# Performance work log

Measured on AMD Instinct MI355X. Metric: run time of the kernel, lower is better.

Reference implementation:

```python
import jax, jax.numpy as jnp
import numpy as np

ALPHA = 0.01  # matches LineFinderLoss(alpha=0.01)


def setup_inputs() -> dict:
    key = jax.random.key(0)
    k1, k2 = jax.random.split(key)
    S = 4096  # square so N == M == S (required for the original code to run)
    # column 4 is used as a probability: log(c) and log(1-c) must be finite
    inp = jax.random.uniform(k1, (S, S), dtype=jnp.float32, minval=1e-4, maxval=1.0 - 1e-4)
    tgt = jax.random.uniform(k2, (S, S), dtype=jnp.float32)
    return {"input": inp, "target": tgt}


def reference(input, target):
    N = input.shape[1]
    M = target.shape[1]
    # pairwise MSE cost over the first two coordinates: cost[n,m] = mean((input[n,:2]-target[m,:2])^2)
    diff = input[:, None, 0:2] - target[None, :, 0:2]  # [N, M, 2]
    cost = jnp.mean(diff * diff, axis=-1)              # [N, M]
    # Hungarian on an NxN cost yields a full assignment; the original code sets
    # X[p,l]=1 for the OUTER PRODUCT of matched row/col index sets, so X == ones
    # deterministically (matching does not affect the output).
    X = jnp.ones((N, M), dtype=input.dtype)
    mse_full = jnp.mean((input - target) ** 2)  # self.mse(input, target), constant over (n,m)
    log_c = jnpp_log = jnp.log(input[:, 4])     # [N]
    log_1mc = jnp.log(1.0 - input[:, 4])        # [N]
    # sum_{n,m} X*(alpha*mse_full - log c_n) - (1-X)*log(1-c_n)
    term = X * (ALPHA * mse_full - log_c[:, None]) - (1.0 - X) * log_1mc[:, None]
    # torch mse_loss(input[:,3], target) broadcasts (S,) against (S,S): elem [i,j] = (input[j,3]-target[i,j])^2
    loss = jnp.sum(term) + jnp.mean((input[:, 3] - target) ** 2)
    return loss, cost
```

## Files before the change

### kernel.cpp

```cpp
#include <hip/hip_runtime.h>

#define SDIM 4096
#define ALPHA 0.01f
#define WS_LOG 8
#define WS_ARR 128
#define WS_PART (WS_ARR + 5 * SDIM)


__global__ void k_gather(const float* __restrict__ inp, const float* __restrict__ tgt,
                         float* __restrict__ ws) {
    int n = blockIdx.x * 64 + threadIdx.x;
    const float* row = inp + (size_t)n * SDIM;
    const float* trow = tgt + (size_t)n * SDIM;
    float* arr = ws + WS_ARR;

    float v0 = row[0], v1 = row[1], v3 = row[3], v4 = row[4];
    arr[n]            = v0;
    arr[SDIM + n]     = v1;
    arr[2 * SDIM + n] = v3;
    arr[3 * SDIM + n] = trow[0];
    arr[4 * SDIM + n] = trow[1];

    float lg = logf(v4);
    #pragma unroll
    for (int off = 32; off > 0; off >>= 1) lg += __shfl_down(lg, off);
    if (threadIdx.x == 0) ws[WS_LOG + blockIdx.x] = lg;
}

__global__ void __launch_bounds__(256) k_main(const float* __restrict__ inp,
                                              const float* __restrict__ tgt,
                                              const float* __restrict__ ws,
                                              float* __restrict__ out,
                                              float* __restrict__ wpart) {
    __shared__ float s1[4], s2[4];
    const float* c0 = ws + WS_ARR;
    const float* c1 = c0 + SDIM;
    const float* c3 = c0 + 2 * SDIM;
    const float* t0 = c0 + 3 * SDIM;
    const float* t1 = c0 + 4 * SDIM;

    int n = blockIdx.x;
    int t = threadIdx.x;
    const float* irow = inp + (size_t)n * SDIM;
    const float* trow = tgt + (size_t)n * SDIM;
    float* orow = out + 1 + (size_t)n * SDIM;

    float4 vi[4], vt[4];
    #pragma unroll
    for (int k = 0; k < 4; ++k) {
        int col = (k * 256 + t) * 4;
        vi[k] = *(const float4*)(irow + col);
        vt[k] = *(const float4*)(trow + col);
    }
    float4 vc[4], w0[4], w1[4];
    #pragma unroll
    for (int k = 0; k < 4; ++k) {
        int col = (k * 256 + t) * 4;
        vc[k] = *(const float4*)(c3 + col);
        w0[k] = *(const float4*)(t0 + col);
        w1[k] = *(const float4*)(t1 + col);
    }
    float a0 = c0[n];
    float b0 = c1[n];

    float a1 = 0.0f, a2 = 0.0f;
    #pragma unroll
    for (int k = 0; k < 4; ++k) {
        int col = (k * 256 + t) * 4;
        float d, e0, e1;
        d = vi[k].x - vt[k].x; a1 += d * d;
        d = vi[k].y - vt[k].y; a1 += d * d;
        d = vi[k].z - vt[k].z; a1 += d * d;
        d = vi[k].w - vt[k].w; a1 += d * d;
        d = vc[k].x - vt[k].x; a2 += d * d;
        d = vc[k].y - vt[k].y; a2 += d * d;
        d = vc[k].z - vt[k].z; a2 += d * d;
        d = vc[k].w - vt[k].w; a2 += d * d;
        e0 = a0 - w0[k].x; e1 = b0 - w1[k].x; orow[col + 0] = 0.5f * (e0 * e0 + e1 * e1);
        e0 = a0 - w0[k].y; e1 = b0 - w1[k].y; orow[col + 1] = 0.5f * (e0 * e0 + e1 * e1);
        e0 = a0 - w0[k].z; e1 = b0 - w1[k].z; orow[col + 2] = 0.5f * (e0 * e0 + e1 * e1);
        e0 = a0 - w0[k].w; e1 = b0 - w1[k].w; orow[col + 3] = 0.5f * (e0 * e0 + e1 * e1);
    }

    #pragma unroll
    for (int off = 32; off > 0; off >>= 1) {
        a1 += __shfl_down(a1, off);
        a2 += __shfl_down(a2, off);
    }
    int wave = t >> 6;
    if ((t & 63) == 0) { s1[wave] = a1; s2[wave] = a2; }
    __syncthreads();
    if (t == 0) {
        wpart[n]        = s1[0] + s1[1] + s1[2] + s1[3];
        wpart[SDIM + n] = s2[0] + s2[1] + s2[2] + s2[3];
    }
}

__global__ void k_final(const float* __restrict__ ws, float* __restrict__ out) {
    __shared__ float s1[4], s2[4];
    float a1 = 0.0f, a2 = 0.0f;
    const float* wpart = ws + WS_PART;
    for (int i = threadIdx.x; i < SDIM; i += 256) {
        a1 += wpart[i];
        a2 += wpart[SDIM + i];
    }
    #pragma unroll
    for (int off = 32; off > 0; off >>= 1) {
        a1 += __shfl_down(a1, off);
        a2 += __shfl_down(a2, off);
    }
    int wave = threadIdx.x >> 6;
    if ((threadIdx.x & 63) == 0) { s1[wave] = a1; s2[wave] = a2; }
    __syncthreads();
    if (threadIdx.x == 0) {
        float sum_sq = s1[0] + s1[1] + s1[2] + s1[3];
        float sum3   = s2[0] + s2[1] + s2[2] + s2[3];
        float slog = 0.0f;
        #pragma unroll
        for (int i = 0; i < 64; ++i) slog += ws[WS_LOG + i];
        out[0] = ALPHA * sum_sq - (float)SDIM * slog
               + sum3 * (1.0f / ((float)SDIM * (float)SDIM));
    }
}

extern "C" void kernel_launch(void* const* d_in, const int* in_sizes, int n_in,
                              void* d_out, int out_size, void* d_ws, size_t ws_size,
                              hipStream_t stream) {
    const float* inp = (const float*)d_in[0];
    const float* tgt = (const float*)d_in[1];
    float* out = (float*)d_out;
    float* ws  = (float*)d_ws;

    k_gather<<<64, 64, 0, stream>>>(inp, tgt, ws);
    k_main<<<SDIM, 256, 0, stream>>>(inp, tgt, ws, out, ws + WS_PART);
    k_final<<<1, 256, 0, stream>>>(ws, out);
}
```

Baseline: 181.4 us.

## Split main kernel into reduction blocks and aligned float4 cost-row writer blocks

Replaces the single per-row kernel with a grid that interleaves reduction blocks (every third block, reading input/target in large strided float4 chunks) and cost-writer blocks. The writer blocks store the output shifted by one element so each row is written with aligned float4 stores. This handles the off-by-one offset of the cost matrix within the output buffer by pre-shifting the target columns in the gather kernel and patching the boundary elements. The aim is to replace scalar unaligned stores with vector stores and to separate read-heavy work from write-heavy work. The cost is more complex indexing and special-case boundary handling.

New measurement: 185.4 us. 1.02x slower.

```diff
diff --git a/kernel.cpp b/kernel.cpp
--- a/kernel.cpp
+++ b/kernel.cpp
@@ -5,12 +5,13 @@
 #define WS_LOG 8
 #define WS_ARR 128
 #define WS_PART (WS_ARR + 5 * SDIM)
+#define NRED 2048
 
 
 __global__ void k_gather(const float* __restrict__ inp, const float* __restrict__ tgt,
                          float* __restrict__ ws) {
     int n = blockIdx.x * 64 + threadIdx.x;
-    const float* row = inp + (size_t)n * SDIM;
+    const float* row  = inp + (size_t)n * SDIM;
     const float* trow = tgt + (size_t)n * SDIM;
     float* arr = ws + WS_ARR;
 
@@ -18,8 +19,9 @@
     arr[n]            = v0;
     arr[SDIM + n]     = v1;
     arr[2 * SDIM + n] = v3;
-    arr[3 * SDIM + n] = trow[0];
-    arr[4 * SDIM + n] = trow[1];
+    int ns = (n + 1) & (SDIM - 1);
+    arr[3 * SDIM + ns] = trow[0];
+    arr[4 * SDIM + ns] = trow[1];
 
     float lg = logf(v4);
     #pragma unroll
@@ -27,72 +29,86 @@
     if (threadIdx.x == 0) ws[WS_LOG + blockIdx.x] = lg;
 }
 
-__global__ void __launch_bounds__(256) k_main(const float* __restrict__ inp,
-                                              const float* __restrict__ tgt,
-                                              const float* __restrict__ ws,
-                                              float* __restrict__ out,
-                                              float* __restrict__ wpart) {
+__global__ void __launch_bounds__(256) k_fused(const float* __restrict__ inp,
+                                               const float* __restrict__ tgt,
+                                               const float* __restrict__ ws,
+                                               float* __restrict__ out,
+                                               float* __restrict__ wpart) {
     __shared__ float s1[4], s2[4];
+    int bid = blockIdx.x;
+    int t = threadIdx.x;
     const float* c0 = ws + WS_ARR;
-    const float* c1 = c0 + SDIM;
-    const float* c3 = c0 + 2 * SDIM;
-    const float* t0 = c0 + 3 * SDIM;
-    const float* t1 = c0 + 4 * SDIM;
 
-    int n = blockIdx.x;
-    int t = threadIdx.x;
-    const float* irow = inp + (size_t)n * SDIM;
-    const float* trow = tgt + (size_t)n * SDIM;
-    float* orow = out + 1 + (size_t)n * SDIM;
-
-    float4 vi[4], vt[4];
-    #pragma unroll
-    for (int k = 0; k < 4; ++k) {
-        int col = (k * 256 + t) * 4;
-        vi[k] = *(const float4*)(irow + col);
-        vt[k] = *(const float4*)(trow + col);
-    }
-    float4 vc[4], w0[4], w1[4];
-    #pragma unroll
-    for (int k = 0; k < 4; ++k) {
-        int col = (k * 256 + t) * 4;
-        vc[k] = *(const float4*)(c3 + col);
-        w0[k] = *(const float4*)(t0 + col);
-        w1[k] = *(const float4*)(t1 + col);
-    }
-    float a0 = c0[n];
-    float b0 = c1[n];
-
-    float a1 = 0.0f, a2 = 0.0f;
-    #pragma unroll
-    for (int k = 0; k < 4; ++k) {
-        int col = (k * 256 + t) * 4;
-        float d, e0, e1;
-        d = vi[k].x - vt[k].x; a1 += d * d;
-        d = vi[k].y - vt[k].y; a1 += d * d;
-        d = vi[k].z - vt[k].z; a1 += d * d;
-        d = vi[k].w - vt[k].w; a1 += d * d;
-        d = vc[k].x - vt[k].x; a2 += d * d;
-        d = vc[k].y - vt[k].y; a2 += d * d;
-        d = vc[k].z - vt[k].z; a2 += d * d;
-        d = vc[k].w - vt[k].w; a2 += d * d;
-        e0 = a0 - w0[k].x; e1 = b0 - w1[k].x; orow[col + 0] = 0.5f * (e0 * e0 + e1 * e1);
-        e0 = a0 - w0[k].y; e1 = b0 - w1[k].y; orow[col + 1] = 0.5f * (e0 * e0 + e1 * e1);
-        e0 = a0 - w0[k].z; e1 = b0 - w1[k].z; orow[col + 2] = 0.5f * (e0 * e0 + e1 * e1);
-        e0 = a0 - w0[k].w; e1 = b0 - w1[k].w; orow[col + 3] = 0.5f * (e0 * e0 + e1 * e1);
-    }
-
-    #pragma unroll
-    for (int off = 32; off > 0; off >>= 1) {
-        a1 += __shfl_down(a1, off);
-        a2 += __shfl_down(a2, off);
-    }
-    int wave = t >> 6;
-    if ((t & 63) == 0) { s1[wave] = a1; s2[wave] = a2; }
-    __syncthreads();
-    if (t == 0) {
-        wpart[n]        = s1[0] + s1[1] + s1[2] + s1[3];
-        wpart[SDIM + n] = s2[0] + s2[1] + s2[2] + s2[3];
+    if (bid % 3 == 0) {
+        int r = bid / 3;
+        const float4* inp4 = (const float4*)inp;
+        const float4* tgt4 = (const float4*)tgt;
+        const float4* c34  = (const float4*)(c0 + 2 * SDIM);
+        int base = r * 256 + t;
+        float a1 = 0.f, a2 = 0.f, b1 = 0.f, b2 = 0.f;
+        #pragma unroll
+        for (int i = 0; i < 8; i += 2) {
+            int ua = base + i * 524288;
+            int ub = ua + 524288;
+            float4 ia = inp4[ua], ta = tgt4[ua], ca = c34[ua & 1023];
+            float4 ib = inp4[ub], tb = tgt4[ub], cb = c34[ub & 1023];
+            float d;
+            d = ia.x - ta.x; a1 += d * d;  d = ia.y - ta.y; a1 += d * d;
+            d = ia.z - ta.z; a1 += d * d;  d = ia.w - ta.w; a1 += d * d;
+            d = ca.x - ta.x; a2 += d * d;  d = ca.y - ta.y; a2 += d * d;
+            d = ca.z - ta.z; a2 += d * d;  d = ca.w - ta.w; a2 += d * d;
+            d = ib.x - tb.x; b1 += d * d;  d = ib.y - tb.y; b1 += d * d;
+            d = ib.z - tb.z; b1 += d * d;  d = ib.w - tb.w; b1 += d * d;
+            d = cb.x - tb.x; b2 += d * d;  d = cb.y - tb.y; b2 += d * d;
+            d = cb.z - tb.z; b2 += d * d;  d = cb.w - tb.w; b2 += d * d;
+        }
+        a1 += b1; a2 += b2;
+        #pragma unroll
+        for (int off = 32; off > 0; off >>= 1) {
+            a1 += __shfl_down(a1, off);
+            a2 += __shfl_down(a2, off);
+        }
+        int wave = t >> 6;
+        if ((t & 63) == 0) { s1[wave] = a1; s2[wave] = a2; }
+        __syncthreads();
+        if (t == 0) {
+            wpart[r]        = s1[0] + s1[1] + s1[2] + s1[3];
+            wpart[NRED + r] = s2[0] + s2[1] + s2[2] + s2[3];
+        }
+    } else {
+        int n = 2 * (bid / 3) + (bid % 3) - 1;
+        const float* c1 = c0 + SDIM;
+        const float4* u04 = (const float4*)(c0 + 3 * SDIM);
+        const float4* u14 = (const float4*)(c0 + 4 * SDIM);
+        float a0 = c0[n], b0 = c1[n];
+        float4* orow4 = (float4*)(out + (size_t)n * SDIM);
+        #pragma unroll
+        for (int k = 0; k < 4; ++k) {
+            int j = k * 256 + t;
+            float4 U0 = u04[j], U1 = u14[j];
+            float e0, e1;
+            float4 v;
+            e0 = a0 - U0.x; e1 = b0 - U1.x; v.x = 0.5f * (e0 * e0 + e1 * e1);
+            e0 = a0 - U0.y; e1 = b0 - U1.y; v.y = 0.5f * (e0 * e0 + e1 * e1);
+            e0 = a0 - U0.z; e1 = b0 - U1.z; v.z = 0.5f * (e0 * e0 + e1 * e1);
+            e0 = a0 - U0.w; e1 = b0 - U1.w; v.w = 0.5f * (e0 * e0 + e1 * e1);
+            if (j == 0) {
+                if (n == 0) {
+                    v.x = 0.0f;
+                } else {
+                    float ap = c0[n - 1], bp = c1[n - 1];
+                    e0 = ap - U0.x; e1 = bp - U1.x;
+                    v.x = 0.5f * (e0 * e0 + e1 * e1);
+                }
+            }
+            orow4[j] = v;
+        }
+        if (n == SDIM - 1 && t == 255) {
+            const float* u0 = c0 + 3 * SDIM;
+            const float* u1 = c0 + 4 * SDIM;
+            float e0 = a0 - u0[0], e1 = b0 - u1[0];
+            out[(size_t)SDIM * SDIM] = 0.5f * (e0 * e0 + e1 * e1);
+        }
     }
 }
 
@@ -100,9 +116,9 @@
     __shared__ float s1[4], s2[4];
     float a1 = 0.0f, a2 = 0.0f;
     const float* wpart = ws + WS_PART;
-    for (int i = threadIdx.x; i < SDIM; i += 256) {
+    for (int i = threadIdx.x; i < NRED; i += 256) {
         a1 += wpart[i];
-        a2 += wpart[SDIM + i];
+        a2 += wpart[NRED + i];
     }
     #pragma unroll
     for (int off = 32; off > 0; off >>= 1) {
@@ -132,6 +148,6 @@
     float* ws  = (float*)d_ws;
 
     k_gather<<<64, 64, 0, stream>>>(inp, tgt, ws);
-    k_main<<<SDIM, 256, 0, stream>>>(inp, tgt, ws, out, ws + WS_PART);
+    k_fused<<<6144, 256, 0, stream>>>(inp, tgt, ws, out, ws + WS_PART);
     k_final<<<1, 256, 0, stream>>>(ws, out);
 }
```
